# Kernel optimization log

Hardware: AMD Instinct MI355X
Metric: run time of the kernel (lower is better)

## Reference

```python
import jax, jax.numpy as jnp
import numpy as np

NUM_CLASSES = 80
MAX_ANCHOR_MATCHES = 10
ALPHA = 0.5
BETA = 6.0
EPSILON = 1e-09
KEPS = 1e-07  # keras.backend.epsilon()
IMG = 640


def make_anchors():
    pts = []
    for stride in (8, 16, 32):
        n = IMG // stride
        xs = (jnp.arange(n, dtype=jnp.float32) + 0.5) * stride
        gy, gx = jnp.meshgrid(xs, xs, indexing='ij')
        pts.append(jnp.stack([gx.reshape(-1), gy.reshape(-1)], axis=-1))
    return jnp.concatenate(pts, axis=0)  # [8400, 2]


def make_boxes(key, shape, max_wh):
    kc, ks = jax.random.split(key)
    cxy = jax.random.uniform(kc, shape) * (IMG - 2.0 * max_wh) + max_wh
    wh = jax.random.uniform(ks, shape) * (max_wh - 4.0) + 4.0
    return jnp.concatenate([cxy - wh / 2.0, cxy + wh / 2.0], axis=-1)


def setup_inputs() -> dict:
    key = jax.random.key(0)
    B, A, C, M = 32, 8400, NUM_CLASSES, 64
    k1, k2, k3, k4 = jax.random.split(key, 4)
    scores = jax.random.uniform(k1, (B, A, C), dtype=jnp.float32)
    decode_bboxes = make_boxes(k2, (B, A, 2), 96.0)
    anchors = make_anchors()
    ground_truth_labels = jax.random.randint(k3, (B, M), 0, C, dtype=jnp.int32)
    ground_truth_bboxes = make_boxes(k4, (B, M, 2), 200.0)
    ground_truth_mask = jax.random.uniform(jax.random.fold_in(key, 7), (B, M, 1)) > 0.2
    return {
        'scores': scores,
        'decode_bboxes': decode_bboxes,
        'anchors': anchors,
        'ground_truth_labels': ground_truth_labels,
        'ground_truth_bboxes': ground_truth_bboxes,
        'ground_truth_mask': ground_truth_mask,
    }


def compute_ciou(boxes1, boxes2):
    # boxes1: [B,M,1,4], boxes2: [B,1,A,4], xyxy -> ciou [B,M,A]
    x_min1, y_min1, x_max1, y_max1 = jnp.split(boxes1, 4, axis=-1)
    x_min2, y_min2, x_max2, y_max2 = jnp.split(boxes2, 4, axis=-1)
    w1 = x_max1 - x_min1
    h1 = y_max1 - y_min1 + KEPS
    w2 = x_max2 - x_min2
    h2 = y_max2 - y_min2 + KEPS
    inter = (jnp.maximum(jnp.minimum(x_max1, x_max2) - jnp.maximum(x_min1, x_min2), 0.0)
             * jnp.maximum(jnp.minimum(y_max1, y_max2) - jnp.maximum(y_min1, y_min2), 0.0))
    union = w1 * h1 + w2 * h2 - inter + KEPS
    iou = jnp.squeeze(inter / union, -1)
    cw = jnp.maximum(x_max1, x_max2) - jnp.minimum(x_min1, x_min2)
    ch = jnp.maximum(y_max1, y_max2) - jnp.minimum(y_min1, y_min2)
    c2 = cw ** 2 + ch ** 2 + KEPS  # enclosing-box diagonal squared
    rho2 = ((x_min2 + x_max2 - x_min1 - x_max1) ** 2
            + (y_min2 + y_max2 - y_min1 - y_max1) ** 2) / 4.0  # center distance squared
    v = jnp.squeeze((4.0 / np.pi ** 2)
                    * (jnp.arctan(w2 / h2) - jnp.arctan(w1 / h1)) ** 2, -1)
    alpha = v / (v - iou + (1.0 + KEPS))
    return iou - (jnp.squeeze(rho2 / c2, -1) + v * alpha)


def reference(scores, decode_bboxes, anchors, ground_truth_labels,
              ground_truth_bboxes, ground_truth_mask):
    B, A, C = scores.shape
    M = ground_truth_bboxes.shape[1]
    K = MAX_ANCHOR_MATCHES

    # gather predicted class score for each GT label: [B, M, A]
    idx = jnp.maximum(ground_truth_labels[:, None, :], 0).astype(jnp.int32)
    bbox_scores = jnp.take_along_axis(scores, jnp.broadcast_to(idx, (B, A, M)), axis=-1)
    bbox_scores = jnp.transpose(bbox_scores, (0, 2, 1))

    overlaps = compute_ciou(ground_truth_bboxes[:, :, None, :],
                            decode_bboxes[:, None, :, :])  # [B, M, A]

    alignment = (bbox_scores ** ALPHA) * (overlaps ** BETA)
    alignment = jnp.where(ground_truth_mask, alignment, 0.0)
    in_box = jnp.all((ground_truth_bboxes[:, :, None, :2] < anchors)
                     & (ground_truth_bboxes[:, :, None, 2:] > anchors), axis=-1)
    alignment = jnp.where(in_box, alignment, 0.0)

    cand_metrics, cand_idxs = jax.lax.top_k(alignment, K)  # [B, M, K]
    cand_idxs = jnp.where(cand_metrics > 0, cand_idxs, -1)

    # sum of one-hot over K candidates == scatter-add of validity (top_k idxs distinct)
    valid = (cand_idxs >= 0).astype(overlaps.dtype)
    matched = jnp.zeros_like(overlaps).at[
        jnp.arange(B)[:, None, None],
        jnp.arange(M)[None, :, None],
        jnp.clip(cand_idxs, 0),
    ].add(valid)

    overlaps = overlaps * matched
    gt_match = jnp.argmax(overlaps, axis=1).astype(jnp.int32)  # [B, A]
    gt_match_mask = jnp.max(overlaps, axis=1) > 0

    bbox_labels = jnp.take_along_axis(
        ground_truth_bboxes, jnp.broadcast_to(gt_match[:, :, None], (B, A, 4)), axis=1)
    bbox_labels = jnp.where(gt_match_mask[:, :, None], bbox_labels, -1.0)

    class_labels = jnp.take_along_axis(ground_truth_labels, gt_match, axis=1)
    class_labels = jnp.where(gt_match_mask, class_labels, -1)
    class_onehot = jax.nn.one_hot(class_labels.astype(jnp.int32), NUM_CLASSES,
                                  dtype=scores.dtype)

    alignment = alignment * matched
    max_align = jnp.max(alignment, axis=-1, keepdims=True)  # [B, M, 1]
    max_ov = jnp.max(overlaps, axis=-1, keepdims=True)      # [B, M, 1]
    norm_align = jnp.max(alignment * max_ov / (max_align + EPSILON), axis=-2)  # [B, A]
    class_targets = class_onehot * norm_align[:, :, None]

    bbox_labels = jnp.reshape(bbox_labels, (-1, A, 4))
    return (jax.lax.stop_gradient(bbox_labels),
            jax.lax.stop_gradient(class_targets),
            jax.lax.stop_gradient((gt_match > 0).astype(jnp.float32)))
```

## Files before the change

kernel.cpp:

```cpp
#include <hip/hip_runtime.h>
#include <math.h>

#define NCLS 80
#define KTOP 10
#define NB 32
#define NA 8400
#define NM 64
#define F_EPS 1e-9f
#define F_KEPS 1e-7f
#define TPB 256
#define NSLOT 33
#define CAP 1024
#define NCAND (NM * KTOP)

__device__ __forceinline__ float ciou_one(float gx0, float gy0, float gx1, float gy1,
                                          float area1, float atanG, float4 pb)
{
    float w2 = pb.z - pb.x;
    float h2 = pb.w - pb.y + F_KEPS;
    float ix = fminf(gx1, pb.z) - fmaxf(gx0, pb.x);
    float iy = fminf(gy1, pb.w) - fmaxf(gy0, pb.y);
    float inter = fmaxf(ix, 0.f) * fmaxf(iy, 0.f);
    float uni = area1 + w2 * h2 - inter + F_KEPS;
    float iou = inter / uni;
    float cw = fmaxf(gx1, pb.z) - fminf(gx0, pb.x);
    float ch = fmaxf(gy1, pb.w) - fminf(gy0, pb.y);
    float c2 = cw * cw + ch * ch + F_KEPS;
    float dx = pb.x + pb.z - gx0 - gx1;
    float dy = pb.y + pb.w - gy0 - gy1;
    float rho2 = (dx * dx + dy * dy) * 0.25f;
    float dv = atanf(w2 / h2) - atanG;
    const float c4pi2 = 4.0f / (float)(M_PI * M_PI);
    float v = c4pi2 * dv * dv;
    float alpha = v / (v - iou + (1.0f + F_KEPS));
    return iou - (rho2 / c2 + v * alpha);
}

__global__ __launch_bounds__(256) void k_align(const float* __restrict__ scores,
    const float* __restrict__ dbox, const float* __restrict__ anchors,
    const int* __restrict__ gtl, const float* __restrict__ gtb,
    const void* __restrict__ gtm,
    int* __restrict__ cand_idx, float* __restrict__ cand_ov, float* __restrict__ cand_ct)
{
    __shared__ float s_al [CAP];
    __shared__ float s_ovl[CAP];
    __shared__ int   s_pk [CAP];
    __shared__ int   s_n;
    __shared__ int   s_bad;
    __shared__ float s_wv[4];
    __shared__ int   s_wp[4];
    __shared__ int   s_sel[KTOP];
    __shared__ float s_selv[KTOP];
    __shared__ float s_selo[KTOP];
    __shared__ float s_ratio;

    const int bid = blockIdx.x;
    const int bm = (bid & 7) * (NB * NM / 8) + (bid >> 3);
    const int b = bm >> 6;
    const int t = threadIdx.x;
    const int lane = t & 63;

    if (t == 0) { s_bad = 0; s_n = 0; }
    __syncthreads();
    {
        const unsigned int* gw = (const unsigned int*)gtm;
        unsigned int w0 = gw[t];
        unsigned int w1 = gw[t + 256];
        if (w0 > 1u || w1 > 1u) s_bad = 1;
    }
    if (t < KTOP) { s_sel[t] = -1; s_selv[t] = 0.f; s_selo[t] = 0.f; }
    __syncthreads();
    const bool int_mask = (s_bad == 0);

    bool maskv = int_mask ? (((const int*)gtm)[bm] != 0)
                          : (((const unsigned char*)gtm)[bm] != 0);
    if (!maskv) {
        if (t < KTOP) {
            cand_idx[bm * KTOP + t] = -1;
            cand_ov [bm * KTOP + t] = 0.f;
            cand_ct [bm * KTOP + t] = 0.f;
        }
        return;
    }

    const float gx0 = gtb[bm * 4 + 0], gy0 = gtb[bm * 4 + 1];
    const float gx1 = gtb[bm * 4 + 2], gy1 = gtb[bm * 4 + 3];
    const int lbl = max(gtl[bm], 0);
    const float w1 = gx1 - gx0;
    const float h1 = gy1 - gy0 + F_KEPS;
    const float atanG = atanf(w1 / h1);
    const float area1 = w1 * h1;

    const float4* pbv = (const float4*)dbox + (size_t)b * NA;
    const float2* anc = (const float2*)anchors;
    const float*  sb  = scores + (size_t)b * NA * NCLS + lbl;

    for (int k = 0; k < NSLOT; ++k) {
        int a = k * TPB + t;
        float al = 0.f, ov = 0.f;
        if (a < NA) {
            float2 an = anc[a];
            if ((gx0 < an.x) & (gy0 < an.y) & (gx1 > an.x) & (gy1 > an.y)) {
                float4 pb = pbv[a];
                ov = ciou_one(gx0, gy0, gx1, gy1, area1, atanG, pb);
                float sc = sb[(size_t)a * NCLS];
                float t2 = ov * ov;
                al = sqrtf(sc) * (t2 * t2 * t2);
            }
        }
        bool pos = al > 0.f;
        unsigned long long ball = __ballot(pos);
        if (ball) {
            int leader = (int)__builtin_ctzll(ball);
            int cnt = __popcll(ball);
            int base = 0;
            if (lane == leader) base = atomicAdd(&s_n, cnt);
            base = __shfl(base, leader, 64);
            if (pos) {
                int rank = __popcll(ball & ((1ull << lane) - 1ull));
                int slot = base + rank;
                if (slot < CAP) {
                    s_al [slot] = al;
                    s_ovl[slot] = ov;
                    s_pk [slot] = (a << 10) | slot;
                }
            }
        }
    }
    __syncthreads();
    const int n = min(s_n, CAP);

    for (int kk = 0; kk < KTOP; ++kk) {
        float bv = 0.f; int bp = 0x7fffffff;
        for (int slot = t; slot < n; slot += TPB) {
            float v = s_al[slot];
            int  pk = s_pk[slot];
            if (v > bv || (v == bv && pk < bp)) { bv = v; bp = pk; }
        }
        #pragma unroll
        for (int s = 1; s < 64; s <<= 1) {
            float qv = __shfl_xor(bv, s, 64);
            int   qp = __shfl_xor(bp, s, 64);
            if (qv > bv || (qv == bv && qp < bp)) { bv = qv; bp = qp; }
        }
        if (lane == 0) { s_wv[t >> 6] = bv; s_wp[t >> 6] = bp; }
        __syncthreads();
        float wv = s_wv[0]; int wp = s_wp[0];
        #pragma unroll
        for (int w = 1; w < 4; ++w) {
            float v2 = s_wv[w]; int p2 = s_wp[w];
            if (v2 > wv || (v2 == wv && p2 < wp)) { wv = v2; wp = p2; }
        }
        __syncthreads();
        if (wv <= 0.f) break;
        if (t == 0) {
            int slot = wp & (CAP - 1);
            s_sel [kk] = wp >> 10;
            s_selv[kk] = wv;
            s_selo[kk] = s_ovl[slot];
            s_al[slot] = -1.f;
        }
        __syncthreads();
    }
    __syncthreads();

    if (t == 0) {
        float max_al = s_selv[0];
        float max_ov = 0.f;
        for (int k2 = 0; k2 < KTOP; ++k2)
            if (s_sel[k2] >= 0) max_ov = fmaxf(max_ov, s_selo[k2]);
        s_ratio = max_ov / (max_al + F_EPS);
    }
    __syncthreads();
    if (t < KTOP) {
        int id = s_sel[t];
        cand_idx[bm * KTOP + t] = id;
        cand_ov [bm * KTOP + t] = (id >= 0) ? s_selo[t] : 0.f;
        cand_ct [bm * KTOP + t] = (id >= 0) ? s_selv[t] * s_ratio : 0.f;
    }
}

__global__ __launch_bounds__(256) void k_out(const float* __restrict__ gtb,
    const int* __restrict__ gtl,
    const int* __restrict__ cand_idx, const float* __restrict__ cand_ov,
    const float* __restrict__ cand_ct,
    float* __restrict__ out_bbox, float* __restrict__ out_cls,
    float* __restrict__ out_match)
{
    __shared__ int   s_fpk[NCAND];
    __shared__ float s_fov[NCAND];
    __shared__ float s_fct[NCAND];
    __shared__ int   s_fn;
    const int b = blockIdx.y;
    const int a0 = blockIdx.x * 256;
    const int t = threadIdx.x;
    const int a = a0 + t;

    if (t == 0) s_fn = 0;
    __syncthreads();

    for (int i = t; i < NCAND; i += 256) {
        int id = cand_idx[b * NCAND + i];
        unsigned int d = (unsigned int)(id - a0);
        if (d < 256u) {
            int slot = atomicAdd(&s_fn, 1);
            s_fpk[slot] = ((int)d << 6) | (i / KTOP);
            s_fov[slot] = cand_ov[b * NCAND + i];
            s_fct[slot] = cand_ct[b * NCAND + i];
        }
    }

    const int nA = min(256, NA - a0);
    float4* cb = (float4*)(out_cls + ((size_t)b * NA + a0) * NCLS);
    const int nW = nA * NCLS / 4;
    for (int i = t; i < nW; i += 256) cb[i] = make_float4(0.f, 0.f, 0.f, 0.f);

    __syncthreads();
    const int fn = s_fn;

    if (a < NA) {
        unsigned long long mm = 0ull;
        float best_v = -INFINITY; int best_m = NM;
        float normv = 0.f;
        for (int i = 0; i < fn; ++i) {
            int pk = s_fpk[i];
            if ((pk >> 6) == t) {
                int m = pk & 63;
                mm |= (1ull << m);
                float v = s_fov[i];
                if (v > best_v || (v == best_v && m < best_m)) { best_v = v; best_m = m; }
                normv = fmaxf(normv, s_fct[i]);
            }
        }
        unsigned long long inv = ~mm;
        int mz = (inv == 0ull) ? NM : (int)__builtin_ctzll(inv);
        float wv; int wm;
        if (mz < NM) { wv = 0.f; wm = mz; } else { wv = -INFINITY; wm = 0; }
        if (mm != 0ull && (best_v > wv || (best_v == wv && best_m < wm))) {
            wv = best_v; wm = best_m;
        }
        bool matched = wv > 0.f;

        float4 bb = matched ? ((const float4*)gtb)[b * NM + wm]
                            : make_float4(-1.f, -1.f, -1.f, -1.f);
        ((float4*)out_bbox)[(size_t)b * NA + a] = bb;
        out_match[(size_t)b * NA + a] = (wm > 0) ? 1.f : 0.f;
        if (matched) {
            int c = gtl[b * NM + wm];
            if ((unsigned)c < NCLS)
                out_cls[((size_t)b * NA + a) * NCLS + c] = normv;
        }
    }
}

extern "C" void kernel_launch(void* const* d_in, const int* in_sizes, int n_in,
                              void* d_out, int out_size, void* d_ws, size_t ws_size,
                              hipStream_t stream)
{
    const float* scores  = (const float*)d_in[0];
    const float* dbox    = (const float*)d_in[1];
    const float* anchors = (const float*)d_in[2];
    const int*   gtl     = (const int*)d_in[3];
    const float* gtb     = (const float*)d_in[4];
    const void*  gtm     = d_in[5];

    char* p = (char*)d_ws;
    int*   cand_idx = (int*)p;    p += (size_t)NB * NCAND * 4;
    float* cand_ov  = (float*)p;  p += (size_t)NB * NCAND * 4;
    float* cand_ct  = (float*)p;

    float* out_bbox  = (float*)d_out;
    float* out_cls   = out_bbox + (size_t)NB * NA * 4;
    float* out_match = out_cls + (size_t)NB * NA * NCLS;

    k_align<<<NB * NM, 256, 0, stream>>>(
        scores, dbox, anchors, gtl, gtb, gtm,
        cand_idx, cand_ov, cand_ct);
    k_out<<<dim3((NA + 255) / 256, NB), 256, 0, stream>>>(
        gtb, gtl, cand_idx, cand_ov, cand_ct, out_bbox, out_cls, out_match);
}
```

Baseline: 204.5 us.

## Restrict per-GT anchor scan to grid windows covering the GT box

Each GT block no longer loops over all 8400 anchors. It works out, for each of the three stride levels, the range of grid cells that overlap the GT box, then walks only those cells. Anchor centres are recomputed from the cell index and stride instead of being read from the anchors input. This removes most of the iterations, the per-anchor anchor loads and the inside-box tests that always failed. In exchange it assumes the anchors follow the fixed 8/16/32-stride grid, and the order in which candidates are visited changes.

Result: faster. 186.0 us (-9.1%).

```diff
diff --git a/kernel.cpp b/kernel.cpp
--- a/kernel.cpp
+++ b/kernel.cpp
@@ -9,7 +9,6 @@
 #define F_EPS 1e-9f
 #define F_KEPS 1e-7f
 #define TPB 256
-#define NSLOT 33
 #define CAP 1024
 #define NCAND (NM * KTOP)
 
@@ -37,7 +36,7 @@
 }
 
 __global__ __launch_bounds__(256) void k_align(const float* __restrict__ scores,
-    const float* __restrict__ dbox, const float* __restrict__ anchors,
+    const float* __restrict__ dbox,
     const int* __restrict__ gtl, const float* __restrict__ gtb,
     const void* __restrict__ gtm,
     int* __restrict__ cand_idx, float* __restrict__ cand_ov, float* __restrict__ cand_ct)
@@ -92,15 +91,51 @@
     const float area1 = w1 * h1;
 
     const float4* pbv = (const float4*)dbox + (size_t)b * NA;
-    const float2* anc = (const float2*)anchors;
     const float*  sb  = scores + (size_t)b * NA * NCLS + lbl;
 
-    for (int k = 0; k < NSLOT; ++k) {
-        int a = k * TPB + t;
+    int js0, is0, rw0, cnt0, js1, is1, rw1, cnt1, js2, is2, rw2, cnt2;
+    {
+        int jlo, jhi, ilo, ihi, rh;
+        jlo = max(0, (int)floorf(gx0 * 0.125f  - 0.5f) - 1);
+        jhi = min(79, (int)ceilf (gx1 * 0.125f  - 0.5f) + 1);
+        ilo = max(0, (int)floorf(gy0 * 0.125f  - 0.5f) - 1);
+        ihi = min(79, (int)ceilf (gy1 * 0.125f  - 0.5f) + 1);
+        js0 = jlo; is0 = ilo; rw0 = max(0, jhi - jlo + 1); rh = max(0, ihi - ilo + 1);
+        cnt0 = rw0 * rh;
+        jlo = max(0, (int)floorf(gx0 * 0.0625f - 0.5f) - 1);
+        jhi = min(39, (int)ceilf (gx1 * 0.0625f - 0.5f) + 1);
+        ilo = max(0, (int)floorf(gy0 * 0.0625f - 0.5f) - 1);
+        ihi = min(39, (int)ceilf (gy1 * 0.0625f - 0.5f) + 1);
+        js1 = jlo; is1 = ilo; rw1 = max(0, jhi - jlo + 1); rh = max(0, ihi - ilo + 1);
+        cnt1 = rw1 * rh;
+        jlo = max(0, (int)floorf(gx0 * 0.03125f - 0.5f) - 1);
+        jhi = min(19, (int)ceilf (gx1 * 0.03125f - 0.5f) + 1);
+        ilo = max(0, (int)floorf(gy0 * 0.03125f - 0.5f) - 1);
+        ihi = min(19, (int)ceilf (gy1 * 0.03125f - 0.5f) + 1);
+        js2 = jlo; is2 = ilo; rw2 = max(0, jhi - jlo + 1); rh = max(0, ihi - ilo + 1);
+        cnt2 = rw2 * rh;
+    }
+    const int c01 = cnt0 + cnt1;
+    const int total = c01 + cnt2;
+    const int nIter = (total + TPB - 1) / TPB;
+
+    for (int it = 0; it < nIter; ++it) {
+        int f = it * TPB + t;
         float al = 0.f, ov = 0.f;
-        if (a < NA) {
-            float2 an = anc[a];
-            if ((gx0 < an.x) & (gy0 < an.y) & (gx1 > an.x) & (gy1 > an.y)) {
+        int a = 0;
+        if (f < total) {
+            int r, iy, jx, n_, base_;
+            float s_;
+            if (f < cnt0)      { r = f;        iy = r / rw0; jx = r - iy * rw0;
+                                 iy += is0; jx += js0; n_ = 80; base_ = 0;    s_ = 8.f;  }
+            else if (f < c01)  { r = f - cnt0; iy = r / rw1; jx = r - iy * rw1;
+                                 iy += is1; jx += js1; n_ = 40; base_ = 6400; s_ = 16.f; }
+            else               { r = f - c01;  iy = r / rw2; jx = r - iy * rw2;
+                                 iy += is2; jx += js2; n_ = 20; base_ = 8000; s_ = 32.f; }
+            float ax = ((float)jx + 0.5f) * s_;
+            float ay = ((float)iy + 0.5f) * s_;
+            a = base_ + iy * n_ + jx;
+            if ((gx0 < ax) & (gy0 < ay) & (gx1 > ax) & (gy1 > ay)) {
                 float4 pb = pbv[a];
                 ov = ciou_one(gx0, gy0, gx1, gy1, area1, atanG, pb);
                 float sc = sb[(size_t)a * NCLS];
@@ -259,7 +294,6 @@
 {
     const float* scores  = (const float*)d_in[0];
     const float* dbox    = (const float*)d_in[1];
-    const float* anchors = (const float*)d_in[2];
     const int*   gtl     = (const int*)d_in[3];
     const float* gtb     = (const float*)d_in[4];
     const void*  gtm     = d_in[5];
@@ -274,7 +308,7 @@
     float* out_match = out_cls + (size_t)NB * NA * NCLS;
 
     k_align<<<NB * NM, 256, 0, stream>>>(
-        scores, dbox, anchors, gtl, gtb, gtm,
+        scores, dbox, gtl, gtb, gtm,
         cand_idx, cand_ov, cand_ct);
     k_out<<<dim3((NA + 255) / 256, NB), 256, 0, stream>>>(
         gtb, gtl, cand_idx, cand_ov, cand_ct, out_bbox, out_cls, out_match);
```
